# Optimization experiments

Hardware: AMD Instinct MI355X
Metric: run time of the kernel (lower is better)

Reference implementation:

```python
import math
import jax, jax.numpy as jnp
import numpy as np

SCALES = (128.0, 256.0, 512.0)
ASPECT_RATIOS = (0.5, 1.0, 2.0)
NMS_THR = 0.7
PRENMS_K = 6000   # rpn_test_prenms_topk (module built with training=False)
POST_K = 300      # rpn_test_topk
MIN_SIZE = 16.0
DW_CLIP = math.log(1000.0 / 16.0)


def conv2d(x, w, b, pad):
    y = jax.lax.conv_general_dilated(
        x, w, window_strides=(1, 1), padding=[(pad, pad), (pad, pad)],
        dimension_numbers=("NCHW", "OIHW", "NCHW"))
    return y + b[None, :, None, None]


def generate_anchors(im_h, im_w, grid_h, grid_w, dtype):
    stride_h = float(im_h // grid_h)
    stride_w = float(im_w // grid_w)
    ar = jnp.asarray(ASPECT_RATIOS, dtype)
    sc = jnp.asarray(SCALES, dtype)
    h_ratios = jnp.sqrt(ar)
    w_ratios = 1.0 / h_ratios
    hs = (h_ratios[:, None] * sc[None, :]).reshape(-1)   # [A]
    ws = (w_ratios[:, None] * sc[None, :]).reshape(-1)
    base = jnp.round(jnp.stack([-ws, -hs, ws, hs], axis=1) / 2.0)  # [A,4]
    xs = jnp.arange(grid_w, dtype=dtype) * stride_w
    ys = jnp.arange(grid_h, dtype=dtype) * stride_h
    sy, sx = jnp.meshgrid(ys, xs, indexing="ij")
    sx = sx.reshape(-1); sy = sy.reshape(-1)
    shift = jnp.stack([sx, sy, sx, sy], axis=1)           # [HW,4]
    return (shift[:, None, :] + base[None, :, :]).reshape(-1, 4)  # [HW*A,4]


def decode_boxes(pred, anchors):
    # pred, anchors: [N,4] -> decoded [N,4]
    w = anchors[:, 2] - anchors[:, 0]
    h = anchors[:, 3] - anchors[:, 1]
    cx = anchors[:, 0] + 0.5 * w
    cy = anchors[:, 1] + 0.5 * h
    dx, dy = pred[:, 0], pred[:, 1]
    dw = jnp.minimum(pred[:, 2], DW_CLIP)
    dh = jnp.minimum(pred[:, 3], DW_CLIP)
    px = dx * w + cx
    py = dy * h + cy
    pw = jnp.exp(dw) * w
    ph = jnp.exp(dh) * h
    return jnp.stack([px - 0.5 * pw, py - 0.5 * ph, px + 0.5 * pw, py + 0.5 * ph], axis=1)


def nms_keep(boxes, valid, thr):
    # boxes assumed sorted by descending score; sequential greedy NMS.
    N = boxes.shape[0]
    area = (boxes[:, 2] - boxes[:, 0]) * (boxes[:, 3] - boxes[:, 1])
    idx = jnp.arange(N)

    def body(i, keep):
        b = jax.lax.dynamic_slice(boxes, (i, 0), (1, 4))[0]
        x1 = jnp.maximum(b[0], boxes[:, 0])
        y1 = jnp.maximum(b[1], boxes[:, 1])
        x2 = jnp.minimum(b[2], boxes[:, 2])
        y2 = jnp.minimum(b[3], boxes[:, 3])
        inter = jnp.clip(x2 - x1, 0.0) * jnp.clip(y2 - y1, 0.0)
        iou = inter / (area[i] + area - inter)
        suppress = (iou > thr) & (idx > i) & keep[i]
        return keep & ~suppress

    return jax.lax.fori_loop(0, N, body, valid)


def rpn_forward(image, feat, rpn_conv_w, rpn_conv_b, cls_w, cls_b, bbox_w, bbox_b):
    rpn_feat = jax.nn.relu(conv2d(feat, rpn_conv_w, rpn_conv_b, pad=1))
    cls_scores = conv2d(rpn_feat, cls_w, cls_b, pad=0)       # [B,A,H,W]
    box_pred = conv2d(rpn_feat, bbox_w, bbox_b, pad=0)       # [B,4A,H,W]
    B, A, H, W = cls_scores.shape
    im_h, im_w = image.shape[-2], image.shape[-1]
    anchors = generate_anchors(im_h, im_w, H, W, feat.dtype)  # [HWA,4]

    cls_flat = jnp.transpose(cls_scores, (0, 2, 3, 1)).reshape(-1)              # [B*H*W*A]
    pred = jnp.transpose(box_pred.reshape(B, A, 4, H, W), (0, 3, 4, 1, 2)).reshape(-1, 4)
    proposals = decode_boxes(pred, anchors)                   # [N,4]

    scores = jax.nn.sigmoid(cls_flat)
    top_scores, top_idx = jax.lax.top_k(scores, PRENMS_K)
    props = proposals[top_idx]                                # [K,4]
    # clamp to image boundary
    props = jnp.stack([
        jnp.clip(props[:, 0], 0.0, float(im_w)),
        jnp.clip(props[:, 1], 0.0, float(im_h)),
        jnp.clip(props[:, 2], 0.0, float(im_w)),
        jnp.clip(props[:, 3], 0.0, float(im_h))], axis=1)
    w = props[:, 2] - props[:, 0]
    h = props[:, 3] - props[:, 1]
    valid = (w >= MIN_SIZE) & (h >= MIN_SIZE)
    keep = nms_keep(props, valid, NMS_THR)                    # already score-sorted
    masked = jnp.where(keep, top_scores, -jnp.inf)
    final_scores, sel = jax.lax.top_k(masked, POST_K)
    final_boxes = props[sel]
    ok = jnp.isfinite(final_scores)
    final_boxes = jnp.where(ok[:, None], final_boxes, 0.0)
    final_scores = jnp.where(ok, final_scores, 0.0)
    return jnp.concatenate([final_boxes, final_scores[:, None]], axis=1)  # [POST_K,5]


def setup_inputs() -> dict:
    key = jax.random.key(0)
    ks = jax.random.split(key, 6)
    C, H, W, A = 256, 128, 128, 9
    IMH = IMW = 1024
    std = 0.01
    return {
        "image": jax.random.normal(ks[0], (1, 3, IMH, IMW), jnp.float32),
        "feat": jax.random.normal(ks[1], (1, C, H, W), jnp.float32),
        "rpn_conv_w": jax.random.normal(ks[2], (C, C, 3, 3), jnp.float32) * std,
        "rpn_conv_b": jnp.zeros((C,), jnp.float32),
        "cls_w": jax.random.normal(ks[3], (A, C, 1, 1), jnp.float32) * std,
        "cls_b": jnp.zeros((A,), jnp.float32),
        "bbox_w": jax.random.normal(ks[4], (4 * A, C, 1, 1), jnp.float32) * std,
        "bbox_b": jnp.zeros((4 * A,), jnp.float32),
    }


def reference(image, feat, rpn_conv_w, rpn_conv_b, cls_w, cls_b, bbox_w, bbox_b):
    return rpn_forward(image, feat, rpn_conv_w, rpn_conv_b, cls_w, cls_b, bbox_w, bbox_b)
```

## Files before the change

### kernel.cpp

```cpp
#include <hip/hip_runtime.h>

#define HW 128
#define NPIX 16384
#define CIN 256
#define NSC 147456
#define PRENMS 6000
#define POSTK 300
#define DW_CLIP_F 4.135166556742356f
#define MW 96
typedef unsigned long long ull;

__global__ void zero_kernel(unsigned* __restrict__ p, int n) {
    int i = blockIdx.x * 256 + threadIdx.x;
    if (i < n) p[i] = 0u;
}

__global__ void wt_kernel(const float* __restrict__ w, float* __restrict__ wt) {
    int i = blockIdx.x * 256 + threadIdx.x;
    if (i < 2304 * 256) {
        int k = i >> 8, co = i & 255;
        wt[i] = w[co * 2304 + k];
    }
}

__global__ __launch_bounds__(256) void conv3x3_half_kernel(
    const float* __restrict__ feat, const float* __restrict__ wt,
    float* __restrict__ part)
{
    __shared__ float in_s[16 * 340];
    const int tx = threadIdx.x;
    const int ty = threadIdx.y;
    const int x0 = blockIdx.x * 32;
    const int y0 = blockIdx.y * 8;
    const int h  = blockIdx.z >> 3;
    const int co0 = (blockIdx.z & 7) << 5;
    const int tid = ty * 32 + tx;

    const int yy1 = tid / 34, xx1 = tid - yy1 * 34;
    const int t2 = tid + 256;
    const int yy2 = t2 / 34, xx2 = t2 - yy2 * 34;
    const int gy1 = y0 + yy1 - 1, gx1 = x0 + xx1 - 1;
    const int gy2 = y0 + yy2 - 1, gx2 = x0 + xx2 - 1;
    const bool p1 = ((unsigned)gy1 < 128u) && ((unsigned)gx1 < 128u);
    const bool p2 = (tid < 84) && ((unsigned)gy2 < 128u) && ((unsigned)gx2 < 128u);
    const int a1 = p1 ? (gy1 * 128 + gx1) : 0;
    const int a2 = p2 ? (gy2 * 128 + gx2) : 0;

    float acc[32];
#pragma unroll
    for (int i = 0; i < 32; ++i) acc[i] = 0.f;

    const float* fh = feat + h * 128 * NPIX;
    const float* wh = wt + h * 128 * 9 * 256;

    for (int s = 0; s < 8; ++s) {
        __syncthreads();
        const float* fbase = fh + s * 16 * NPIX;
#pragma unroll
        for (int ci = 0; ci < 16; ++ci) {
            float t = fbase[ci * NPIX + a1];
            in_s[ci * 340 + tid] = p1 ? t : 0.f;
        }
        if (tid < 84) {
#pragma unroll
            for (int ci = 0; ci < 16; ++ci) {
                float t = fbase[ci * NPIX + a2];
                in_s[ci * 340 + 256 + tid] = p2 ? t : 0.f;
            }
        }
        __syncthreads();
        const float* ws0 = wh + s * 16 * 9 * 256 + co0;
#pragma unroll 2
        for (int ci = 0; ci < 16; ++ci) {
            const float* wrow = ws0 + ci * 9 * 256;
#pragma unroll
            for (int t = 0; t < 9; ++t) {
                const int ky = t / 3, kx = t - ky * 3;
                float v = in_s[ci * 340 + (ty + ky) * 34 + (tx + kx)];
                const float* wp = wrow + t * 256;
#pragma unroll
                for (int co = 0; co < 32; ++co)
                    acc[co] = fmaf(v, wp[co], acc[co]);
            }
        }
    }
    float* po = part + h * (CIN * NPIX) + co0 * NPIX + (y0 + ty) * 128 + (x0 + tx);
#pragma unroll
    for (int co = 0; co < 32; ++co)
        po[co * NPIX] = acc[co];
}

__global__ __launch_bounds__(256) void combine_kernel(
    float* __restrict__ part, const float* __restrict__ b)
{
    const int i = blockIdx.x * 256 + threadIdx.x;
    float4 a = ((const float4*)part)[i];
    float4 c = ((const float4*)(part + CIN * NPIX))[i];
    float bias = b[i >> 12];
    float4 r;
    r.x = fmaxf(a.x + c.x + bias, 0.f);
    r.y = fmaxf(a.y + c.y + bias, 0.f);
    r.z = fmaxf(a.z + c.z + bias, 0.f);
    r.w = fmaxf(a.w + c.w + bias, 0.f);
    ((float4*)part)[i] = r;
}

__global__ __launch_bounds__(64) void heads_kernel(
    const float* __restrict__ rf,
    const float* __restrict__ cls_w, const float* __restrict__ cls_b,
    const float* __restrict__ bbox_w, const float* __restrict__ bbox_b,
    float* __restrict__ scores, float* __restrict__ bb)
{
    __shared__ float wl[256][48];
    const int tid = threadIdx.x;
    for (int e = tid; e < 256 * 45; e += 64) {
        int ci = e / 45, s = e - ci * 45;
        wl[ci][s] = (s < 9) ? cls_w[s * CIN + ci] : bbox_w[(s - 9) * CIN + ci];
    }
    __syncthreads();

    const int p = blockIdx.x * 64 + tid;
    float acc[45];
#pragma unroll
    for (int i = 0; i < 45; ++i) acc[i] = 0.f;

#pragma unroll 2
    for (int ci = 0; ci < CIN; ++ci) {
        float v = rf[ci * NPIX + p];
        const float4* wr = (const float4*)&wl[ci][0];
#pragma unroll
        for (int q = 0; q < 11; ++q) {
            float4 w4 = wr[q];
            acc[q * 4 + 0] = fmaf(v, w4.x, acc[q * 4 + 0]);
            acc[q * 4 + 1] = fmaf(v, w4.y, acc[q * 4 + 1]);
            acc[q * 4 + 2] = fmaf(v, w4.z, acc[q * 4 + 2]);
            acc[q * 4 + 3] = fmaf(v, w4.w, acc[q * 4 + 3]);
        }
        acc[44] = fmaf(v, wl[ci][44], acc[44]);
    }
#pragma unroll
    for (int a = 0; a < 9; ++a) {
        float s = acc[a] + cls_b[a];
        scores[p * 9 + a] = 1.0f / (1.0f + expf(-s));
    }
#pragma unroll
    for (int c = 0; c < 36; ++c) {
        bb[c * NPIX + p] = acc[9 + c] + bbox_b[c];
    }
}

__global__ __launch_bounds__(1024) void hist1_kernel(const float* __restrict__ scores,
                                                     unsigned* __restrict__ hist1) {
    __shared__ unsigned h[16384];
    const int tid = threadIdx.x;
    for (int i = tid; i < 16384; i += 1024) h[i] = 0u;
    __syncthreads();
    for (int i = blockIdx.x * 1024 + tid; i < NSC; i += gridDim.x * 1024) {
        unsigned bits = __float_as_uint(scores[i]);
        atomicAdd(&h[bits >> 16], 1u);
    }
    __syncthreads();
    for (int i = tid; i < 16384; i += 1024) {
        unsigned c = h[i];
        if (c) atomicAdd(&hist1[i], c);
    }
}

__global__ __launch_bounds__(1024) void scan1_kernel(const unsigned* __restrict__ hist,
                                                     unsigned* __restrict__ meta) {
    __shared__ unsigned ssum[1024];
    const int t = threadIdx.x;
    unsigned local[16];
    unsigned s = 0;
#pragma unroll
    for (int i = 0; i < 16; ++i) { local[i] = hist[t * 16 + i]; s += local[i]; }
    ssum[t] = s;
    __syncthreads();
    for (int off = 1; off < 1024; off <<= 1) {
        unsigned v = ssum[t] + ((t + off < 1024) ? ssum[t + off] : 0u);
        __syncthreads();
        ssum[t] = v;
        __syncthreads();
    }
    unsigned run = ssum[t] - s;
#pragma unroll
    for (int i = 15; i >= 0; --i) {
        unsigned nb = run + local[i];
        if (nb >= (unsigned)PRENMS && run < (unsigned)PRENMS) {
            meta[1] = (unsigned)(t * 16 + i);
            meta[2] = run;
        }
        run = nb;
    }
}

__global__ void hist2_kernel(const float* __restrict__ scores, const unsigned* __restrict__ meta,
                             unsigned* __restrict__ hist2) {
    int i = blockIdx.x * 256 + threadIdx.x;
    if (i < NSC) {
        unsigned bits = __float_as_uint(scores[i]);
        if ((bits >> 16) == meta[1]) atomicAdd(&hist2[bits & 0xFFFFu], 1u);
    }
}

__global__ __launch_bounds__(1024) void scan2_kernel(const unsigned* __restrict__ hist2,
                                                     unsigned* __restrict__ meta) {
    __shared__ unsigned ssum[1024];
    const int t = threadIdx.x;
    const unsigned need = (unsigned)PRENMS - meta[2];
    unsigned s = 0;
    for (int i = 0; i < 64; ++i) s += hist2[t * 64 + i];
    ssum[t] = s;
    __syncthreads();
    for (int off = 1; off < 1024; off <<= 1) {
        unsigned v = ssum[t] + ((t + off < 1024) ? ssum[t + off] : 0u);
        __syncthreads();
        ssum[t] = v;
        __syncthreads();
    }
    unsigned run = ssum[t] - s;
    for (int i = 63; i >= 0; --i) {
        unsigned h = hist2[t * 64 + i];
        unsigned nb = run + h;
        if (nb >= need && run < need) {
            meta[3] = (meta[1] << 16) | (unsigned)(t * 64 + i);
        }
        run = nb;
    }
}

__global__ void compact_kernel(const float* __restrict__ scores, unsigned* __restrict__ meta,
                               ull* __restrict__ cand) {
    int i = blockIdx.x * 256 + threadIdx.x;
    unsigned bits = (i < NSC) ? __float_as_uint(scores[i]) : 0u;
    bool pred = (i < NSC) && (bits >= meta[3]);
    ull bal = __ballot(pred);
    int lane = threadIdx.x & 63;
    unsigned cnt = (unsigned)__popcll(bal);
    unsigned base = 0;
    if (lane == 0 && cnt) base = atomicAdd(&meta[0], cnt);
    base = __shfl(base, 0);
    if (pred) {
        unsigned off = (unsigned)__popcll(bal & ((1ull << lane) - 1ull));
        unsigned pos = base + off;
        if (pos < 8192u)
            cand[pos] = ((ull)bits << 32) | (unsigned)(~i);
    }
}

__global__ __launch_bounds__(1024) void sortA_kernel(const ull* __restrict__ cand,
                                                     const unsigned* __restrict__ meta,
                                                     ull* __restrict__ sorted) {
    __shared__ ull keys[2048];
    const int tid = threadIdx.x;
    const int base = blockIdx.x * 2048;
    const int n = min((int)meta[0], 8192);
    for (int i = tid; i < 2048; i += 1024) {
        int g = base + i;
        keys[i] = (g < n) ? cand[g] : (ull)(8191 - g);
    }
    __syncthreads();
    for (int k = 2; k <= 2048; k <<= 1) {
        for (int j = k >> 1; j >= 1; j >>= 1) {
            int s = tid;
            int i = ((s & ~(j - 1)) << 1) | (s & (j - 1));
            int p = i | j;
            ull a = keys[i], c = keys[p];
            bool desc = ((i & k) == 0);
            bool sw = desc ? (a < c) : (a > c);
            if (sw) { keys[i] = c; keys[p] = a; }
            __syncthreads();
        }
    }
    for (int i = tid; i < 2048; i += 1024) sorted[base + i] = keys[i];
}

__global__ __launch_bounds__(256) void merge_kernel(const ull* __restrict__ sorted,
                                                    ull* __restrict__ fin) {
    const int g = blockIdx.x * 256 + threadIdx.x;
    ull x = sorted[g];
    const int c = g >> 11;
    int rank = g & 2047;
#pragma unroll
    for (int cc = 0; cc < 4; ++cc) {
        if (cc == c) continue;
        const ull* arr = sorted + cc * 2048;
        int lo = 0, hi = 2048;
        while (lo < hi) { int mid = (lo + hi) >> 1; if (arr[mid] > x) lo = mid + 1; else hi = mid; }
        rank += lo;
    }
    fin[rank] = x;
}

__global__ __launch_bounds__(64) void decode_kernel(
    const ull* __restrict__ fin, const float* __restrict__ bb,
    float* __restrict__ selbox, float* __restrict__ selsc,
    ull* __restrict__ validbits)
{
    const int r = blockIdx.x * 64 + threadIdx.x;
    int valid = 0;
    if (r < PRENMS) {
        ull key = fin[r];
        unsigned sbits = (unsigned)(key >> 32);
        unsigned idx = ~(unsigned)(key & 0xFFFFFFFFull);
        float score = __uint_as_float(sbits);
        int p = (int)(idx / 9u);
        int a = (int)(idx - (unsigned)p * 9u);
        int y = p >> 7, x = p & 127;
        float d0 = bb[(a * 4 + 0) * NPIX + p];
        float d1 = bb[(a * 4 + 1) * NPIX + p];
        float d2 = bb[(a * 4 + 2) * NPIX + p];
        float d3 = bb[(a * 4 + 3) * NPIX + p];
        int ar_i = a / 3, sc_i = a - ar_i * 3;
        float arv = (ar_i == 0) ? 0.5f : ((ar_i == 1) ? 1.0f : 2.0f);
        float scv = (sc_i == 0) ? 128.f : ((sc_i == 1) ? 256.f : 512.f);
        float hr = sqrtf(arv);
        float wr = 1.0f / hr;
        float hs = hr * scv;
        float wsv = wr * scv;
        float bx1 = rintf(-wsv * 0.5f), by1 = rintf(-hs * 0.5f);
        float bx2 = rintf(wsv * 0.5f),  by2 = rintf(hs * 0.5f);
        float ax1 = x * 8.f + bx1, ay1 = y * 8.f + by1;
        float ax2 = x * 8.f + bx2, ay2 = y * 8.f + by2;
        float wa = ax2 - ax1, ha = ay2 - ay1;
        float cx = ax1 + 0.5f * wa, cy = ay1 + 0.5f * ha;
        float dw = fminf(d2, DW_CLIP_F), dh = fminf(d3, DW_CLIP_F);
        float px = d0 * wa + cx, py = d1 * ha + cy;
        float pw = expf(dw) * wa, ph = expf(dh) * ha;
        float x1 = px - 0.5f * pw, y1 = py - 0.5f * ph;
        float x2 = px + 0.5f * pw, y2 = py + 0.5f * ph;
        x1 = fminf(fmaxf(x1, 0.f), 1024.f);
        y1 = fminf(fmaxf(y1, 0.f), 1024.f);
        x2 = fminf(fmaxf(x2, 0.f), 1024.f);
        y2 = fminf(fmaxf(y2, 0.f), 1024.f);
        float bw = x2 - x1, bh = y2 - y1;
        valid = (bw >= 16.f) && (bh >= 16.f);
        selbox[r * 4 + 0] = x1; selbox[r * 4 + 1] = y1;
        selbox[r * 4 + 2] = x2; selbox[r * 4 + 3] = y2;
        selsc[r] = score;
    }
    ull bal = __ballot(valid);
    if (threadIdx.x == 0) validbits[blockIdx.x] = bal;
}

__global__ __launch_bounds__(256) void maskbuild_kernel(
    const float* __restrict__ selbox, ull* __restrict__ mask)
{
    __shared__ float jb0[64], jb1[64], jb2[64], jb3[64];
    const int jw = blockIdx.y;
    const int tid = threadIdx.x;
    const int i = blockIdx.x * 256 + tid;
    if (jw * 64 + 63 < blockIdx.x * 256) {
        if (i < PRENMS) mask[(size_t)i * MW + jw] = 0ull;
        return;
    }
    if (tid < 64) {
        int j = jw * 64 + tid;
        float x1 = 0.f, y1 = 0.f, x2 = 0.f, y2 = 0.f;
        if (j < PRENMS) {
            x1 = selbox[j * 4 + 0]; y1 = selbox[j * 4 + 1];
            x2 = selbox[j * 4 + 2]; y2 = selbox[j * 4 + 3];
        }
        jb0[tid] = x1; jb1[tid] = y1; jb2[tid] = x2; jb3[tid] = y2;
    }
    __syncthreads();
    if (i >= PRENMS) return;
    const float ix1 = selbox[i * 4 + 0], iy1 = selbox[i * 4 + 1];
    const float ix2 = selbox[i * 4 + 2], iy2 = selbox[i * 4 + 3];
    const float iarea = (ix2 - ix1) * (iy2 - iy1);
    ull word = 0ull;
    for (int b = 0; b < 64; ++b) {
        int j = jw * 64 + b;
        float xx1 = fmaxf(ix1, jb0[b]);
        float yy1 = fmaxf(iy1, jb1[b]);
        float xx2 = fminf(ix2, jb2[b]);
        float yy2 = fminf(iy2, jb3[b]);
        float iw = fmaxf(xx2 - xx1, 0.f);
        float ih = fmaxf(yy2 - yy1, 0.f);
        float inter = iw * ih;
        float jarea = (jb2[b] - jb0[b]) * (jb3[b] - jb1[b]);
        float iou = inter / (iarea + jarea - inter);
        if (j > i && iou > 0.7f) word |= (1ull << b);
    }
    mask[(size_t)i * MW + jw] = word;
}

__global__ __launch_bounds__(64) void nms_scan_kernel(
    const ull* __restrict__ validbits,
    const ull* __restrict__ mask,
    const float* __restrict__ selbox, const float* __restrict__ selsc,
    float* __restrict__ out)
{
    __shared__ int kept[POSTK];
    const int l = threadIdx.x;
    ull supp0 = ~validbits[l];
    ull supp1 = (l < 30) ? ~validbits[64 + l] : ~0ull;
    int nk = 0;
    ull ownrow_next = mask[(size_t)l * MW + 0];
    for (int wi = 0; wi < 94 && nk < POSTK; ++wi) {
        ull ownrow = ownrow_next;
        if (wi < 93) ownrow_next = mask[(size_t)((wi + 1) * 64 + l) * MW + (wi + 1)];
        ull wsup = (wi < 64) ? __shfl(supp0, wi) : __shfl(supp1, wi - 64);
        ull active = ~wsup;
        if (!active) continue;
        ull keptbits = 0ull;
        while (active && nk < POSTK) {
            int b = __builtin_ctzll(active);
            keptbits |= (1ull << b);
            if (l == 0) kept[nk] = wi * 64 + b;
            nk++;
            ull rowb = __shfl(ownrow, b);
            ull gt = (b == 63) ? 0ull : (~0ull << (b + 1));
            active &= gt & ~rowb;
        }
        while (keptbits) {
            int b0 = __builtin_ctzll(keptbits); keptbits &= keptbits - 1;
            int b1 = -1, b2 = -1, b3 = -1;
            if (keptbits) { b1 = __builtin_ctzll(keptbits); keptbits &= keptbits - 1; }
            if (keptbits) { b2 = __builtin_ctzll(keptbits); keptbits &= keptbits - 1; }
            if (keptbits) { b3 = __builtin_ctzll(keptbits); keptbits &= keptbits - 1; }
            const ull* r0 = mask + (size_t)(wi * 64 + b0) * MW;
            ull t0a = r0[l], t0b = (l < 30) ? r0[64 + l] : 0ull;
            ull t1a = 0, t1b = 0, t2a = 0, t2b = 0, t3a = 0, t3b = 0;
            if (b1 >= 0) { const ull* r1 = mask + (size_t)(wi * 64 + b1) * MW; t1a = r1[l]; t1b = (l < 30) ? r1[64 + l] : 0ull; }
            if (b2 >= 0) { const ull* r2 = mask + (size_t)(wi * 64 + b2) * MW; t2a = r2[l]; t2b = (l < 30) ? r2[64 + l] : 0ull; }
            if (b3 >= 0) { const ull* r3 = mask + (size_t)(wi * 64 + b3) * MW; t3a = r3[l]; t3b = (l < 30) ? r3[64 + l] : 0ull; }
            supp0 |= t0a | t1a | t2a | t3a;
            supp1 |= t0b | t1b | t2b | t3b;
        }
    }
    __syncthreads();
    for (int r = l; r < POSTK; r += 64) {
        if (r < nk) {
            int i = kept[r];
            out[r * 5 + 0] = selbox[i * 4 + 0];
            out[r * 5 + 1] = selbox[i * 4 + 1];
            out[r * 5 + 2] = selbox[i * 4 + 2];
            out[r * 5 + 3] = selbox[i * 4 + 3];
            out[r * 5 + 4] = selsc[i];
        } else {
            out[r * 5 + 0] = 0.f; out[r * 5 + 1] = 0.f;
            out[r * 5 + 2] = 0.f; out[r * 5 + 3] = 0.f;
            out[r * 5 + 4] = 0.f;
        }
    }
}

extern "C" void kernel_launch(void* const* d_in, const int* in_sizes, int n_in,
                              void* d_out, int out_size, void* d_ws, size_t ws_size,
                              hipStream_t stream) {
    const float* feat    = (const float*)d_in[1];
    const float* conv_w  = (const float*)d_in[2];
    const float* conv_b  = (const float*)d_in[3];
    const float* cls_w   = (const float*)d_in[4];
    const float* cls_b   = (const float*)d_in[5];
    const float* bbox_w  = (const float*)d_in[6];
    const float* bbox_b  = (const float*)d_in[7];
    float* out = (float*)d_out;

    char* ws = (char*)d_ws;
    float*    part      = (float*)(ws + 0);
    float*    rpn_feat  = part;
    float*    wt        = (float*)(ws + 33554432);
    float*    bb        = (float*)(ws + 35913728);
    float*    scores    = (float*)(ws + 38273024);
    unsigned* hist1     = (unsigned*)(ws + 38862848);
    unsigned* hist2     = (unsigned*)(ws + 38928384);
    unsigned* meta      = (unsigned*)(ws + 39190528);
    ull*      cand      = (ull*)(ws + 39190784);
    ull*      sorted    = (ull*)(ws + 39256320);
    ull*      fin       = (ull*)(ws + 39321856);
    float*    selbox    = (float*)(ws + 39387392);
    float*    selsc    = (float*)(ws + 39483648);
    ull*      validbits = (ull*)(ws + 39507712);
    ull*      mask      = (ull*)(ws + 39508480);

    {
        int nz = 16384 + 65536 + 64;
        zero_kernel<<<(nz + 255) / 256, 256, 0, stream>>>(hist1, nz);
    }
    wt_kernel<<<(2304 * 256 + 255) / 256, 256, 0, stream>>>(conv_w, wt);
    conv3x3_half_kernel<<<dim3(4, 16, 16), dim3(32, 8), 0, stream>>>(feat, wt, part);
    combine_kernel<<<4096, 256, 0, stream>>>(part, conv_b);
    heads_kernel<<<256, 64, 0, stream>>>(rpn_feat, cls_w, cls_b, bbox_w, bbox_b, scores, bb);
    hist1_kernel<<<64, 1024, 0, stream>>>(scores, hist1);
    scan1_kernel<<<1, 1024, 0, stream>>>(hist1, meta);
    hist2_kernel<<<(NSC + 255) / 256, 256, 0, stream>>>(scores, meta, hist2);
    scan2_kernel<<<1, 1024, 0, stream>>>(hist2, meta);
    compact_kernel<<<(NSC + 255) / 256, 256, 0, stream>>>(scores, meta, cand);
    sortA_kernel<<<4, 1024, 0, stream>>>(cand, meta, sorted);
    merge_kernel<<<32, 256, 0, stream>>>(sorted, fin);
    decode_kernel<<<94, 64, 0, stream>>>(fin, bb, selbox, selsc, validbits);
    maskbuild_kernel<<<dim3(24, 94), 256, 0, stream>>>(selbox, mask);
    nms_scan_kernel<<<1, 64, 0, stream>>>(validbits, mask, selbox, selsc, out);
}
```

Baseline: 565.9 us.

## Give each conv wave a private LDS tile and split heads outputs across waves

The 3x3 conv kernel now has each 64-lane wave stage its own 4x34 halo tile per 16-channel slice in a private LDS region. This removes both block-wide __syncthreads per slice, at the cost of redundantly loading overlapping halo rows across waves. The heads kernel moves from 64 to 256 threads per block, with four waves each computing 12 of the 45 output channels for the same pixels. That cuts per-thread registers and raises occupancy, while each pixel's feature values are read four times.

```diff
diff --git a/kernel.cpp b/kernel.cpp
--- a/kernel.cpp
+++ b/kernel.cpp
@@ -23,28 +23,35 @@
     }
 }
 
-__global__ __launch_bounds__(256) void conv3x3_half_kernel(
+__global__ __launch_bounds__(256) void conv3x3_wave_kernel(
     const float* __restrict__ feat, const float* __restrict__ wt,
     float* __restrict__ part)
 {
-    __shared__ float in_s[16 * 340];
-    const int tx = threadIdx.x;
-    const int ty = threadIdx.y;
-    const int x0 = blockIdx.x * 32;
-    const int y0 = blockIdx.y * 8;
-    const int h  = blockIdx.z >> 3;
+    __shared__ float lds[4 * 16 * 136];
+    const int tid  = threadIdx.x;
+    const int w    = tid >> 6;
+    const int lane = tid & 63;
+    const int tx   = lane & 31;
+    const int ry   = lane >> 5;
+    const int x0    = blockIdx.x * 32;
+    const int ybase = blockIdx.y * 8 + w * 2;
+    const int h   = blockIdx.z >> 3;
     const int co0 = (blockIdx.z & 7) << 5;
-    const int tid = ty * 32 + tx;
-
-    const int yy1 = tid / 34, xx1 = tid - yy1 * 34;
-    const int t2 = tid + 256;
-    const int yy2 = t2 / 34, xx2 = t2 - yy2 * 34;
-    const int gy1 = y0 + yy1 - 1, gx1 = x0 + xx1 - 1;
-    const int gy2 = y0 + yy2 - 1, gx2 = x0 + xx2 - 1;
+
+    float* wlds = lds + w * (16 * 136);
+
+    const int e1 = lane,       r1 = e1 / 34, c1 = e1 - r1 * 34;
+    const int e2 = lane + 64,  r2 = e2 / 34, c2 = e2 - r2 * 34;
+    const int e3 = lane + 128, r3 = e3 / 34, c3 = e3 - r3 * 34;
+    const int gy1 = ybase - 1 + r1, gx1 = x0 + c1 - 1;
+    const int gy2 = ybase - 1 + r2, gx2 = x0 + c2 - 1;
+    const int gy3 = ybase - 1 + r3, gx3 = x0 + c3 - 1;
     const bool p1 = ((unsigned)gy1 < 128u) && ((unsigned)gx1 < 128u);
-    const bool p2 = (tid < 84) && ((unsigned)gy2 < 128u) && ((unsigned)gx2 < 128u);
+    const bool p2 = ((unsigned)gy2 < 128u) && ((unsigned)gx2 < 128u);
+    const bool p3 = (lane < 8) && ((unsigned)gy3 < 128u) && ((unsigned)gx3 < 128u);
     const int a1 = p1 ? (gy1 * 128 + gx1) : 0;
     const int a2 = p2 ? (gy2 * 128 + gx2) : 0;
+    const int a3 = p3 ? (gy3 * 128 + gx3) : 0;
 
     float acc[32];
 #pragma unroll
@@ -54,29 +61,30 @@
     const float* wh = wt + h * 128 * 9 * 256;
 
     for (int s = 0; s < 8; ++s) {
-        __syncthreads();
         const float* fbase = fh + s * 16 * NPIX;
 #pragma unroll
         for (int ci = 0; ci < 16; ++ci) {
-            float t = fbase[ci * NPIX + a1];
-            in_s[ci * 340 + tid] = p1 ? t : 0.f;
-        }
-        if (tid < 84) {
+            float t1 = fbase[ci * NPIX + a1];
+            float t2 = fbase[ci * NPIX + a2];
+            wlds[ci * 136 + e1] = p1 ? t1 : 0.f;
+            wlds[ci * 136 + e2] = p2 ? t2 : 0.f;
+        }
+        if (lane < 8) {
 #pragma unroll
             for (int ci = 0; ci < 16; ++ci) {
-                float t = fbase[ci * NPIX + a2];
-                in_s[ci * 340 + 256 + tid] = p2 ? t : 0.f;
+                float t3 = fbase[ci * NPIX + a3];
+                wlds[ci * 136 + e3] = p3 ? t3 : 0.f;
             }
         }
-        __syncthreads();
         const float* ws0 = wh + s * 16 * 9 * 256 + co0;
 #pragma unroll 2
         for (int ci = 0; ci < 16; ++ci) {
             const float* wrow = ws0 + ci * 9 * 256;
+            const float* vbase = wlds + ci * 136 + ry * 34 + tx;
 #pragma unroll
             for (int t = 0; t < 9; ++t) {
                 const int ky = t / 3, kx = t - ky * 3;
-                float v = in_s[ci * 340 + (ty + ky) * 34 + (tx + kx)];
+                float v = vbase[ky * 34 + kx];
                 const float* wp = wrow + t * 256;
 #pragma unroll
                 for (int co = 0; co < 32; ++co)
@@ -84,7 +92,7 @@
             }
         }
     }
-    float* po = part + h * (CIN * NPIX) + co0 * NPIX + (y0 + ty) * 128 + (x0 + tx);
+    float* po = part + h * (CIN * NPIX) + co0 * NPIX + (ybase + ry) * 128 + (x0 + tx);
 #pragma unroll
     for (int co = 0; co < 32; ++co)
         po[co * NPIX] = acc[co];
@@ -105,7 +113,7 @@
     ((float4*)part)[i] = r;
 }
 
-__global__ __launch_bounds__(64) void heads_kernel(
+__global__ __launch_bounds__(256) void heads_kernel(
     const float* __restrict__ rf,
     const float* __restrict__ cls_w, const float* __restrict__ cls_b,
     const float* __restrict__ bbox_w, const float* __restrict__ bbox_b,
@@ -113,39 +121,39 @@
 {
     __shared__ float wl[256][48];
     const int tid = threadIdx.x;
-    for (int e = tid; e < 256 * 45; e += 64) {
-        int ci = e / 45, s = e - ci * 45;
-        wl[ci][s] = (s < 9) ? cls_w[s * CIN + ci] : bbox_w[(s - 9) * CIN + ci];
-    }
-    __syncthreads();
-
-    const int p = blockIdx.x * 64 + tid;
-    float acc[45];
-#pragma unroll
-    for (int i = 0; i < 45; ++i) acc[i] = 0.f;
-
-#pragma unroll 2
+    for (int e = tid; e < 256 * 48; e += 256) {
+        int ci = e / 48, s = e - ci * 48;
+        wl[ci][s] = (s < 9) ? cls_w[s * CIN + ci]
+                  : (s < 45) ? bbox_w[(s - 9) * CIN + ci] : 0.f;
+    }
+    __syncthreads();
+
+    const int lane = tid & 63;
+    const int sg   = tid >> 6;
+    const int p    = blockIdx.x * 64 + lane;
+    const int s0   = sg * 12;
+    const int ns   = (sg == 3) ? 9 : 12;
+
+    float acc[12];
+#pragma unroll
+    for (int i = 0; i < 12; ++i) acc[i] = 0.f;
+
+#pragma unroll 4
     for (int ci = 0; ci < CIN; ++ci) {
         float v = rf[ci * NPIX + p];
-        const float4* wr = (const float4*)&wl[ci][0];
-#pragma unroll
-        for (int q = 0; q < 11; ++q) {
-            float4 w4 = wr[q];
-            acc[q * 4 + 0] = fmaf(v, w4.x, acc[q * 4 + 0]);
-            acc[q * 4 + 1] = fmaf(v, w4.y, acc[q * 4 + 1]);
-            acc[q * 4 + 2] = fmaf(v, w4.z, acc[q * 4 + 2]);
-            acc[q * 4 + 3] = fmaf(v, w4.w, acc[q * 4 + 3]);
-        }
-        acc[44] = fmaf(v, wl[ci][44], acc[44]);
-    }
-#pragma unroll
-    for (int a = 0; a < 9; ++a) {
-        float s = acc[a] + cls_b[a];
-        scores[p * 9 + a] = 1.0f / (1.0f + expf(-s));
-    }
-#pragma unroll
-    for (int c = 0; c < 36; ++c) {
-        bb[c * NPIX + p] = acc[9 + c] + bbox_b[c];
+        const float* wr = &wl[ci][s0];
+#pragma unroll
+        for (int j = 0; j < 12; ++j)
+            acc[j] = fmaf(v, wr[j], acc[j]);
+    }
+    for (int j = 0; j < ns; ++j) {
+        int s = s0 + j;
+        if (s < 9) {
+            float sc = acc[j] + cls_b[s];
+            scores[p * 9 + s] = 1.0f / (1.0f + expf(-sc));
+        } else {
+            bb[(s - 9) * NPIX + p] = acc[j] + bbox_b[s - 9];
+        }
     }
 }
 
@@ -471,7 +479,7 @@
     ull*      sorted    = (ull*)(ws + 39256320);
     ull*      fin       = (ull*)(ws + 39321856);
     float*    selbox    = (float*)(ws + 39387392);
-    float*    selsc    = (float*)(ws + 39483648);
+    float*    selsc     = (float*)(ws + 39483648);
     ull*      validbits = (ull*)(ws + 39507712);
     ull*      mask      = (ull*)(ws + 39508480);
 
@@ -480,9 +488,9 @@
         zero_kernel<<<(nz + 255) / 256, 256, 0, stream>>>(hist1, nz);
     }
     wt_kernel<<<(2304 * 256 + 255) / 256, 256, 0, stream>>>(conv_w, wt);
-    conv3x3_half_kernel<<<dim3(4, 16, 16), dim3(32, 8), 0, stream>>>(feat, wt, part);
+    conv3x3_wave_kernel<<<dim3(4, 16, 16), 256, 0, stream>>>(feat, wt, part);
     combine_kernel<<<4096, 256, 0, stream>>>(part, conv_b);
-    heads_kernel<<<256, 64, 0, stream>>>(rpn_feat, cls_w, cls_b, bbox_w, bbox_b, scores, bb);
+    heads_kernel<<<256, 256, 0, stream>>>(rpn_feat, cls_w, cls_b, bbox_w, bbox_b, scores, bb);
     hist1_kernel<<<64, 1024, 0, stream>>>(scores, hist1);
     scan1_kernel<<<1, 1024, 0, stream>>>(hist1, meta);
     hist2_kernel<<<(NSC + 255) / 256, 256, 0, stream>>>(scores, meta, hist2);
```

Measured after the change: 562.9 us. No clear change (-0.5%).
